# Kernel tuning notes

Measured on AMD Instinct MI355X. Metric: run time of the kernel, lower is better.

## Reference

```python
import jax, jax.numpy as jnp
import numpy as np

N_HEADS = 16
THETA = 10000.0

def rotate_half(x):
    x1, x2 = jnp.split(x, 2, axis=-1)
    return jnp.concatenate((-x2, x1), axis=-1)

def setup_inputs() -> dict:
    key = jax.random.key(0)
    k1, k2, k3 = jax.random.split(key, 3)
    B, T, C = 4, 2048, 2048
    x = jax.random.normal(k1, (B, T, C), dtype=jnp.float32)
    # torch Linear weights: y = x @ W.T
    wqkv = jax.random.normal(k2, (3 * C, C), dtype=jnp.float32) * (1.0 / np.sqrt(C))
    w_out = jax.random.normal(k3, (C, C), dtype=jnp.float32) * (1.0 / np.sqrt(C))
    return {"x": x, "wqkv": wqkv, "w_out": w_out}

def reference(x, wqkv, w_out):
    B, T, C = x.shape
    H = N_HEADS
    hd = C // H
    scale = 1.0 / np.sqrt(hd)

    qkv = x @ wqkv.T                               # [B, T, 3C]
    q, k, v = jnp.split(qkv, 3, axis=-1)
    q = q.reshape(B, T, H, hd).transpose(0, 2, 1, 3)  # [B, H, T, hd]
    k = k.reshape(B, T, H, hd).transpose(0, 2, 1, 3)
    v = v.reshape(B, T, H, hd).transpose(0, 2, 1, 3)

    # rotary embedding (kv_len == T, no cache)
    inv_freq = 1.0 / (THETA ** (jnp.arange(0, hd, 2, dtype=jnp.float32) / hd))
    t = jnp.arange(T, dtype=jnp.float32)
    freqs = jnp.einsum("i,j->ij", t, inv_freq)     # [T, hd/2]
    emb = jnp.concatenate((freqs, freqs), axis=-1) # [T, hd]
    cos = jnp.cos(emb)[None, None, :, :]
    sin = jnp.sin(emb)[None, None, :, :]
    q = q * cos + rotate_half(q) * sin
    k = k * cos + rotate_half(k) * sin

    scores = jnp.einsum("bhqd,bhkd->bhqk", q, k) * scale
    causal = jnp.triu(jnp.ones((T, T), dtype=bool), k=1)
    scores = jnp.where(causal[None, None], -jnp.inf, scores)
    attn = jax.nn.softmax(scores, axis=-1)
    out = jnp.einsum("bhqk,bhkd->bhqd", attn, v)   # [B, H, T, hd]
    out = out.transpose(0, 2, 1, 3).reshape(B, T, C)
    output = out @ w_out.T
    return (output, k, v)
```

## Files before the change

### kernel.cpp

```cpp
#include <hip/hip_runtime.h>

#define B_ 4
#define T_ 2048
#define C_ 2048
#define H_ 16
#define HD_ 128
#define BT_ (B_*T_)
#define N3_ (3*C_)

typedef unsigned short u16;
typedef unsigned int u32;
using short8 = __attribute__((ext_vector_type(8))) short;
using f32x4  = __attribute__((ext_vector_type(4))) float;

__device__ __forceinline__ u16 f2bf(float f) {
  union { float f; u32 u; } v; v.f = f;
  u32 r = v.u + 0x7FFFu + ((v.u >> 16) & 1u);
  return (u16)(r >> 16);
}
__device__ __forceinline__ float bf2f(u16 u) {
  union { u32 u; float f; } v; v.u = ((u32)u) << 16;
  return v.f;
}
__device__ __forceinline__ void gload_lds16(const void* g, void* l) {
  __builtin_amdgcn_global_load_lds((const __attribute__((address_space(1))) void*)g,
                                   (__attribute__((address_space(3))) void*)l, 16, 0, 0);
}

__global__ __launch_bounds__(256) void cast_f2b_kernel(const float* __restrict__ in,
                                                       u16* __restrict__ out, int n4) {
  int i = blockIdx.x * 256 + threadIdx.x;
  if (i >= n4) return;
  float4 v = ((const float4*)in)[i];
  ushort4 o;
  o.x = f2bf(v.x); o.y = f2bf(v.y); o.z = f2bf(v.z); o.w = f2bf(v.w);
  ((ushort4*)out)[i] = o;
}

__global__ __launch_bounds__(256) void rope_table_kernel(float* __restrict__ cosb,
                                                         float* __restrict__ sinb) {
  int i = blockIdx.x * 256 + threadIdx.x;
  int t = i >> 6, d = i & 63;
  float inv = powf(10000.0f, -(float)d / 64.0f);
  float ang = (float)t * inv;
  cosb[i] = cosf(ang);
  sinb[i] = sinf(ang);
}

__global__ __launch_bounds__(256) void rope_apply_kernel(const u16* __restrict__ qkv,
    const float* __restrict__ cosb, const float* __restrict__ sinb,
    u16* __restrict__ qb, u16* __restrict__ kbb,
    float* __restrict__ kout, float* __restrict__ vout) {
  int gid = blockIdx.x * 256 + threadIdx.x;
  int d = gid & 63;
  int h = (gid >> 6) & 15;
  int t = (gid >> 10) & 2047;
  int b = gid >> 21;
  const u16* row = qkv + (size_t)(b * T_ + t) * N3_;
  int base = h * HD_ + d;
  const float SCALE = 0.08838834764831845f;
  float q0 = bf2f(row[base]);
  float q1 = bf2f(row[base + 64]);
  float k0 = bf2f(row[C_ + base]);
  float k1 = bf2f(row[C_ + base + 64]);
  float v0 = bf2f(row[2*C_ + base]);
  float v1 = bf2f(row[2*C_ + base + 64]);
  float c = cosb[t * 64 + d], s = sinb[t * 64 + d];
  size_t o = ((size_t)((b * H_ + h) * T_ + t)) * HD_ + d;
  qb[o]        = f2bf((q0 * c - q1 * s) * SCALE);
  qb[o + 64]   = f2bf((q1 * c + q0 * s) * SCALE);
  float kr0 = k0 * c - k1 * s;
  float kr1 = k1 * c + k0 * s;
  kout[o]      = kr0;
  kout[o + 64] = kr1;
  kbb[o]       = f2bf(kr0);
  kbb[o + 64]  = f2bf(kr1);
  vout[o]      = v0;
  vout[o + 64] = v1;
}

__global__ __launch_bounds__(256) void vt_kernel(const u16* __restrict__ qkvb,
                                                 u16* __restrict__ vtb) {
  __shared__ u16 tile[64][72];
  int bid = blockIdx.x;
  int dh = bid & 1, tt = (bid >> 1) & 31, bh = bid >> 6;
  int b = bh >> 4, h = bh & 15;
  int tid = threadIdx.x;
  int tr = tid >> 2, tc = tid & 3;
  const u16* src = qkvb + (size_t)(b*T_ + tt*64 + tr) * N3_ + 2*C_ + h*HD_ + dh*64 + tc*16;
  short8 v0 = *(const short8*)src;
  short8 v1 = *(const short8*)(src + 8);
  #pragma unroll
  for (int j = 0; j < 8; ++j) {
    tile[tr][tc*16 + j]     = (u16)v0[j];
    tile[tr][tc*16 + 8 + j] = (u16)v1[j];
  }
  __syncthreads();
  int dr = tid >> 2, c2 = tid & 3;
  short8 o0, o1;
  #pragma unroll
  for (int j = 0; j < 8; ++j) {
    o0[j] = (short)tile[c2*16 + j][dr];
    o1[j] = (short)tile[c2*16 + 8 + j][dr];
  }
  u16* dst = vtb + ((size_t)bh * HD_ + dh*64 + dr) * T_ + tt*64 + c2*16;
  *(short8*)dst = o0;
  *(short8*)(dst + 8) = o1;
}

template<int OUT_BF16>
__global__ __launch_bounds__(512, 2) void gemm8p_kernel(const u16* __restrict__ A,
    const u16* __restrict__ Bw, void* __restrict__ Cout, int M, int N, int K, int ntx) {
  extern __shared__ u16 ldsx[];
  int lin = blockIdx.x;
  int cpx = gridDim.x >> 3;
  int wg = (lin & 7) * cpx + (lin >> 3);
  int mtile = wg / ntx, ntile = wg - mtile * ntx;
  int tid = threadIdx.x, w = tid >> 6, l = tid & 63;
  int lr = l & 15, lg = l >> 4;
  int wr = w >> 2, wc = w & 3;
  const u16* Abase = A + (size_t)mtile * 256 * K;
  const u16* Bbase = Bw + (size_t)ntile * 256 * K;

  int goff[2], ldsoff[2];
  #pragma unroll
  for (int j = 0; j < 2; ++j) {
    int s = (j*8 + w)*64 + l;
    int row = (s >> 5)*8 + (s & 7);
    int c = (s & 31) >> 3;
    goff[j] = row * K + c*8;
    ldsoff[j] = (j*8 + w) * 512;
  }
  int bbyte[4], abyte[2][4];
  #pragma unroll
  for (int n = 0; n < 4; ++n) {
    int r = wc*64 + n*16 + lr;
    bbyte[n] = ((r & ~7) << 6) + (lg << 7) + ((r & 7) << 4);
  }
  #pragma unroll
  for (int mq = 0; mq < 2; ++mq)
    #pragma unroll
    for (int m = 0; m < 4; ++m) {
      int r = wr*128 + mq*64 + m*16 + lr;
      abyte[mq][m] = ((r & ~7) << 6) + (lg << 7) + ((r & 7) << 4);
    }

  f32x4 acc[8][4];
  #pragma unroll
  for (int mi = 0; mi < 8; ++mi)
    #pragma unroll
    for (int n = 0; n < 4; ++n) acc[mi][n] = (f32x4){0.f,0.f,0.f,0.f};

  const int NT = K >> 5;
  #pragma unroll
  for (int t0 = 0; t0 < 3; ++t0) {
    const u16* ga = Abase + t0*32;
    const u16* gb = Bbase + t0*32;
    u16* la = ldsx + (size_t)t0 * 16384;
    #pragma unroll
    for (int j = 0; j < 2; ++j) gload_lds16(ga + goff[j], la + ldsoff[j]);
    #pragma unroll
    for (int j = 0; j < 2; ++j) gload_lds16(gb + goff[j], la + 8192 + ldsoff[j]);
  }
  asm volatile("s_waitcnt vmcnt(8)" ::: "memory");
  __builtin_amdgcn_s_barrier();

  for (int t = 0; t < NT; ++t) {
    const char* Al = (const char*)(ldsx + (size_t)(t & 3) * 16384);
    const char* Bl = Al + 16384;
    int tp = t + 3;
    bool st = tp < NT;
    u16* lp = ldsx + (size_t)(tp & 3) * 16384;
    if (st) {
      const u16* ga = Abase + tp*32;
      #pragma unroll
      for (int j = 0; j < 2; ++j) gload_lds16(ga + goff[j], lp + ldsoff[j]);
    }
    short8 bf[4], af[4];
    #pragma unroll
    for (int n = 0; n < 4; ++n) bf[n] = *(const short8*)(Bl + bbyte[n]);
    #pragma unroll
    for (int m = 0; m < 4; ++m) af[m] = *(const short8*)(Al + abyte[0][m]);
    __builtin_amdgcn_s_setprio(1);
    #pragma unroll
    for (int m = 0; m < 4; ++m)
      #pragma unroll
      for (int n = 0; n < 4; ++n)
        acc[m][n] = __builtin_amdgcn_mfma_f32_16x16x32_bf16(af[m], bf[n], acc[m][n], 0, 0, 0);
    __builtin_amdgcn_s_setprio(0);
    __builtin_amdgcn_s_barrier();
    if (st) {
      const u16* gb = Bbase + tp*32;
      #pragma unroll
      for (int j = 0; j < 2; ++j) gload_lds16(gb + goff[j], lp + 8192 + ldsoff[j]);
    }
    #pragma unroll
    for (int m = 0; m < 4; ++m) af[m] = *(const short8*)(Al + abyte[1][m]);
    __builtin_amdgcn_s_setprio(1);
    #pragma unroll
    for (int m = 0; m < 4; ++m)
      #pragma unroll
      for (int n = 0; n < 4; ++n)
        acc[4+m][n] = __builtin_amdgcn_mfma_f32_16x16x32_bf16(af[m], bf[n], acc[4+m][n], 0, 0, 0);
    __builtin_amdgcn_s_setprio(0);
    if (t + 1 < NT) {
      if (t + 3 < NT)      asm volatile("s_waitcnt vmcnt(8)" ::: "memory");
      else if (t + 2 < NT) asm volatile("s_waitcnt vmcnt(4)" ::: "memory");
      else                 asm volatile("s_waitcnt vmcnt(0)" ::: "memory");
    }
    __builtin_amdgcn_s_barrier();
  }
  #pragma unroll
  for (int mi = 0; mi < 8; ++mi)
    #pragma unroll
    for (int n = 0; n < 4; ++n)
      #pragma unroll
      for (int r = 0; r < 4; ++r) {
        int grow = mtile*256 + wr*128 + mi*16 + lg*4 + r;
        int gcol = ntile*256 + wc*64 + n*16 + lr;
        float v = acc[mi][n][r];
        if (OUT_BF16) ((u16*)Cout)[(size_t)grow * N + gcol] = f2bf(v);
        else          ((float*)Cout)[(size_t)grow * N + gcol] = v;
      }
}

struct TileSt {
  short8 aq[4];
  f32x4 oacc[8];
  float m_run[4];
  float l_run[4];
};

__device__ __forceinline__ void stage_kv(const u16* kpl, const u16* vpl, int kt,
                                         u16* Kd, u16* Vd, int w, int l) {
  const u16* kTile = kpl + (size_t)kt * 64 * HD_;
  int ktOff = kt * 64;
  #pragma unroll
  for (int j = 0; j < 4; ++j) {
    int s = (j*4 + w)*64 + l;
    int g = s ^ ((s >> 4) & 7);
    gload_lds16(kTile + (g >> 4)*HD_ + (g & 15)*8, (char*)Kd + (j*4 + w)*1024);
    int g2 = s ^ ((s >> 3) & 7);
    gload_lds16(vpl + (size_t)(g2 >> 3)*T_ + ktOff + (g2 & 7)*8, (char*)Vd + (j*4 + w)*1024);
  }
}

__device__ __forceinline__ void attn_tile(TileSt& st, const u16* Kl, const u16* Vl,
                                          char* Pw, bool diag, int lr, int lg, int w) {
  f32x4 s_acc[4];
  #pragma unroll
  for (int ct = 0; ct < 4; ++ct) s_acc[ct] = (f32x4){0.f, 0.f, 0.f, 0.f};
  __builtin_amdgcn_s_setprio(1);
  #pragma unroll
  for (int kg = 0; kg < 4; ++kg) {
    #pragma unroll
    for (int ct = 0; ct < 4; ++ct) {
      int krow = ct*16 + lr;
      int kbyte = (krow*256 + (kg*32 + lg*8)*2) ^ ((krow & 7) << 4);
      short8 bk = *(const short8*)((const char*)Kl + kbyte);
      s_acc[ct] = __builtin_amdgcn_mfma_f32_16x16x32_bf16(st.aq[kg], bk, s_acc[ct], 0, 0, 0);
    }
  }
  __builtin_amdgcn_s_setprio(0);
  float p[4][4];
  #pragma unroll
  for (int ct = 0; ct < 4; ++ct)
    #pragma unroll
    for (int r = 0; r < 4; ++r) {
      float sv = s_acc[ct][r];
      if (diag && (ct*16 + lr) > (w*16 + lg*4 + r)) sv = -INFINITY;
      p[ct][r] = sv;
    }
  float fac[4];
  #pragma unroll
  for (int r = 0; r < 4; ++r) {
    float mx = fmaxf(fmaxf(p[0][r], p[1][r]), fmaxf(p[2][r], p[3][r]));
    #pragma unroll
    for (int off = 1; off < 16; off <<= 1) mx = fmaxf(mx, __shfl_xor(mx, off));
    float mn = fmaxf(st.m_run[r], mx);
    fac[r] = __expf(st.m_run[r] - mn);
    st.m_run[r] = mn;
    float ls = 0.f;
    #pragma unroll
    for (int ct = 0; ct < 4; ++ct) { float pv = __expf(p[ct][r] - mn); p[ct][r] = pv; ls += pv; }
    #pragma unroll
    for (int off = 1; off < 16; off <<= 1) ls += __shfl_xor(ls, off);
    st.l_run[r] = st.l_run[r] * fac[r] + ls;
  }
  #pragma unroll
  for (int dt = 0; dt < 8; ++dt)
    #pragma unroll
    for (int r = 0; r < 4; ++r) st.oacc[dt][r] *= fac[r];
  #pragma unroll
  for (int ct = 0; ct < 4; ++ct)
    #pragma unroll
    for (int r = 0; r < 4; ++r) {
      int prow = lg*4 + r;
      int pb = (prow*128 + (ct*16 + lr)*2) ^ ((prow & 7) << 4);
      *(u16*)(Pw + pb) = f2bf(p[ct][r]);
    }
  asm volatile("s_waitcnt lgkmcnt(0)" ::: "memory");
  __builtin_amdgcn_sched_barrier(0);
  short8 pa[2];
  #pragma unroll
  for (int kk = 0; kk < 2; ++kk) {
    int pb = (lr*128 + (kk*32 + lg*8)*2) ^ ((lr & 7) << 4);
    pa[kk] = *(const short8*)(Pw + pb);
  }
  __builtin_amdgcn_s_setprio(1);
  #pragma unroll
  for (int dt = 0; dt < 8; ++dt) {
    #pragma unroll
    for (int kk = 0; kk < 2; ++kk) {
      int vrow = dt*16 + lr;
      int vbyte = (vrow*128 + (kk*32 + lg*8)*2) ^ ((vrow & 7) << 4);
      short8 bv = *(const short8*)((const char*)Vl + vbyte);
      st.oacc[dt] = __builtin_amdgcn_mfma_f32_16x16x32_bf16(pa[kk], bv, st.oacc[dt], 0, 0, 0);
    }
  }
  __builtin_amdgcn_s_setprio(0);
}

__device__ __forceinline__ void write_out(TileSt& st, u16* __restrict__ ao,
                                          int b, int h, int qbase, int lr, int lg, int w) {
  float invl[4];
  #pragma unroll
  for (int r = 0; r < 4; ++r) invl[r] = 1.0f / st.l_run[r];
  #pragma unroll
  for (int dt = 0; dt < 8; ++dt)
    #pragma unroll
    for (int r = 0; r < 4; ++r) {
      int t = qbase + w*16 + lg*4 + r;
      int col = h*HD_ + dt*16 + lr;
      ao[(size_t)(b * T_ + t) * C_ + col] = f2bf(st.oacc[dt][r] * invl[r]);
    }
}

__global__ __launch_bounds__(256, 2) void attn_kernel(const u16* __restrict__ qb,
    const u16* __restrict__ kb, const u16* __restrict__ vtb, u16* __restrict__ ao) {
  __shared__ u16 Kl[2][64 * 128];
  __shared__ u16 Vl[2][128 * 64];
  __shared__ u16 Pl[4][16 * 64];
  int bid0 = blockIdx.x;
  int bid = (bid0 & 7) * 128 + (bid0 >> 3);
  int bh = bid >> 4, pr = bid & 15;
  int lo = pr, hi = 31 - pr;
  int b = bh >> 4, h = bh & 15;
  int tid = threadIdx.x, w = tid >> 6, l = tid & 63;
  int lr = l & 15, lg = l >> 4;
  const u16* qptr = qb + (size_t)bh * T_ * HD_;
  const u16* kpl  = kb + (size_t)bh * T_ * HD_;
  const u16* vpl  = vtb + (size_t)bh * HD_ * T_;
  char* Pw = (char*)&Pl[w][0];

  TileSt stL, stH;
  #pragma unroll
  for (int kg = 0; kg < 4; ++kg) {
    stL.aq[kg] = *(const short8*)(qptr + (size_t)(lo*64 + w*16 + lr) * HD_ + kg*32 + lg*8);
    stH.aq[kg] = *(const short8*)(qptr + (size_t)(hi*64 + w*16 + lr) * HD_ + kg*32 + lg*8);
  }
  #pragma unroll
  for (int dt = 0; dt < 8; ++dt) {
    stL.oacc[dt] = (f32x4){0.f, 0.f, 0.f, 0.f};
    stH.oacc[dt] = (f32x4){0.f, 0.f, 0.f, 0.f};
  }
  #pragma unroll
  for (int r = 0; r < 4; ++r) {
    stL.m_run[r] = -INFINITY; stH.m_run[r] = -INFINITY;
    stL.l_run[r] = 0.f;       stH.l_run[r] = 0.f;
  }

  stage_kv(kpl, vpl, 0, &Kl[0][0], &Vl[0][0], w, l);
  __syncthreads();
  int cur = 0;
  for (int kt = 0; kt <= hi; ++kt) {
    if (kt < hi) stage_kv(kpl, vpl, kt + 1, &Kl[cur ^ 1][0], &Vl[cur ^ 1][0], w, l);
    attn_tile(stH, &Kl[cur][0], &Vl[cur][0], Pw, kt == hi, lr, lg, w);
    if (kt <= lo) attn_tile(stL, &Kl[cur][0], &Vl[cur][0], Pw, kt == lo, lr, lg, w);
    __syncthreads();
    cur ^= 1;
  }
  write_out(stH, ao, b, h, hi*64, lr, lg, w);
  write_out(stL, ao, b, h, lo*64, lr, lg, w);
}

extern "C" void kernel_launch(void* const* d_in, const int* in_sizes, int n_in,
                              void* d_out, int out_size, void* d_ws, size_t ws_size,
                              hipStream_t stream) {
  const float* x     = (const float*)d_in[0];
  const float* wqkv  = (const float*)d_in[1];
  const float* w_out = (const float*)d_in[2];
  float* out = (float*)d_out;

  char* ws = (char*)d_ws;
  size_t off = 0;
  u16* xb    = (u16*)(ws + off); off += (size_t)BT_ * C_ * 2;
  u16* wqkvb = (u16*)(ws + off); off += (size_t)N3_ * C_ * 2;
  u16* woutb = (u16*)(ws + off); off += (size_t)C_ * C_ * 2;
  u16* qkvb  = (u16*)(ws + off); off += (size_t)BT_ * N3_ * 2;
  u16* qbf   = (u16*)(ws + off); off += (size_t)BT_ * C_ * 2;
  u16* aob   = (u16*)(ws + off); off += (size_t)BT_ * C_ * 2;
  u16* kbb   = (u16*)(ws + off); off += (size_t)BT_ * C_ * 2;
  u16* vtb   = (u16*)(ws + off); off += (size_t)BT_ * C_ * 2;
  float* cosb = (float*)(ws + off); off += (size_t)T_ * 64 * 4;
  float* sinb = (float*)(ws + off); off += (size_t)T_ * 64 * 4;

  float* kout = out + (size_t)BT_ * C_;
  float* vout = out + 2 * (size_t)BT_ * C_;

  hipFuncSetAttribute((const void*)gemm8p_kernel<1>,
                      hipFuncAttributeMaxDynamicSharedMemorySize, 131072);
  hipFuncSetAttribute((const void*)gemm8p_kernel<0>,
                      hipFuncAttributeMaxDynamicSharedMemorySize, 131072);

  cast_f2b_kernel<<<(BT_*C_/4)/256, 256, 0, stream>>>(x, xb, BT_*C_/4);
  cast_f2b_kernel<<<(N3_*C_/4)/256, 256, 0, stream>>>(wqkv, wqkvb, N3_*C_/4);
  cast_f2b_kernel<<<(C_*C_/4)/256, 256, 0, stream>>>(w_out, woutb, C_*C_/4);
  rope_table_kernel<<<(T_*64)/256, 256, 0, stream>>>(cosb, sinb);
  gemm8p_kernel<1><<<(N3_/256)*(BT_/256), 512, 131072, stream>>>(xb, wqkvb, qkvb, BT_, N3_, C_, N3_/256);
  rope_apply_kernel<<<(B_*T_*H_*64)/256, 256, 0, stream>>>(qkvb, cosb, sinb, qbf, kbb, kout, vout);
  vt_kernel<<<B_*H_*(T_/64)*2, 256, 0, stream>>>(qkvb, vtb);
  attn_kernel<<<B_*H_*16, 256, 0, stream>>>(qbf, kbb, vtb, aob);
  gemm8p_kernel<0><<<(C_/256)*(BT_/256), 512, 131072, stream>>>(aob, woutb, out, BT_, C_, C_, C_/256);
}
```

Measured before the change: 572.6 us.

## Prefetch next K-tile LDS fragments into registers and drop mid-loop barrier

```diff
diff --git a/kernel.cpp b/kernel.cpp
--- a/kernel.cpp
+++ b/kernel.cpp
@@ -162,53 +162,67 @@
     #pragma unroll
     for (int j = 0; j < 2; ++j) gload_lds16(gb + goff[j], la + 8192 + ldsoff[j]);
   }
-  asm volatile("s_waitcnt vmcnt(8)" ::: "memory");
+  asm volatile("s_waitcnt vmcnt(4)" ::: "memory");
   __builtin_amdgcn_s_barrier();
 
+  short8 bf[4], af0[4];
+  {
+    const char* Al0 = (const char*)ldsx;
+    #pragma unroll
+    for (int n = 0; n < 4; ++n) bf[n] = *(const short8*)(Al0 + 16384 + bbyte[n]);
+    #pragma unroll
+    for (int m = 0; m < 4; ++m) af0[m] = *(const short8*)(Al0 + abyte[0][m]);
+  }
+
+  #pragma unroll 2
   for (int t = 0; t < NT; ++t) {
-    const char* Al = (const char*)(ldsx + (size_t)(t & 3) * 16384);
-    const char* Bl = Al + 16384;
+    const char* Al  = (const char*)(ldsx + (size_t)(t & 3) * 16384);
+    const char* Aln = (const char*)(ldsx + (size_t)((t+1) & 3) * 16384);
     int tp = t + 3;
     bool st = tp < NT;
     u16* lp = ldsx + (size_t)(tp & 3) * 16384;
+    short8 af1[4], bfn[4], afn[4];
     if (st) {
       const u16* ga = Abase + tp*32;
       #pragma unroll
       for (int j = 0; j < 2; ++j) gload_lds16(ga + goff[j], lp + ldsoff[j]);
     }
-    short8 bf[4], af[4];
-    #pragma unroll
-    for (int n = 0; n < 4; ++n) bf[n] = *(const short8*)(Bl + bbyte[n]);
-    #pragma unroll
-    for (int m = 0; m < 4; ++m) af[m] = *(const short8*)(Al + abyte[0][m]);
+    #pragma unroll
+    for (int m = 0; m < 4; ++m) af1[m] = *(const short8*)(Al + abyte[1][m]);
     __builtin_amdgcn_s_setprio(1);
     #pragma unroll
     for (int m = 0; m < 4; ++m)
       #pragma unroll
       for (int n = 0; n < 4; ++n)
-        acc[m][n] = __builtin_amdgcn_mfma_f32_16x16x32_bf16(af[m], bf[n], acc[m][n], 0, 0, 0);
+        acc[m][n] = __builtin_amdgcn_mfma_f32_16x16x32_bf16(af0[m], bf[n], acc[m][n], 0, 0, 0);
     __builtin_amdgcn_s_setprio(0);
-    __builtin_amdgcn_s_barrier();
     if (st) {
       const u16* gb = Bbase + tp*32;
       #pragma unroll
       for (int j = 0; j < 2; ++j) gload_lds16(gb + goff[j], lp + 8192 + ldsoff[j]);
     }
-    #pragma unroll
-    for (int m = 0; m < 4; ++m) af[m] = *(const short8*)(Al + abyte[1][m]);
+    if (t + 1 < NT) {
+      #pragma unroll
+      for (int n = 0; n < 4; ++n) bfn[n] = *(const short8*)(Aln + 16384 + bbyte[n]);
+      #pragma unroll
+      for (int m = 0; m < 4; ++m) afn[m] = *(const short8*)(Aln + abyte[0][m]);
+    }
     __builtin_amdgcn_s_setprio(1);
     #pragma unroll
     for (int m = 0; m < 4; ++m)
       #pragma unroll
       for (int n = 0; n < 4; ++n)
-        acc[4+m][n] = __builtin_amdgcn_mfma_f32_16x16x32_bf16(af[m], bf[n], acc[4+m][n], 0, 0, 0);
+        acc[4+m][n] = __builtin_amdgcn_mfma_f32_16x16x32_bf16(af1[m], bf[n], acc[4+m][n], 0, 0, 0);
     __builtin_amdgcn_s_setprio(0);
+    if (t >= NT - 3) { asm volatile("s_waitcnt vmcnt(0)" ::: "memory"); }
+    else             { asm volatile("s_waitcnt vmcnt(4)" ::: "memory"); }
+    __builtin_amdgcn_s_barrier();
     if (t + 1 < NT) {
-      if (t + 3 < NT)      asm volatile("s_waitcnt vmcnt(8)" ::: "memory");
-      else if (t + 2 < NT) asm volatile("s_waitcnt vmcnt(4)" ::: "memory");
-      else                 asm volatile("s_waitcnt vmcnt(0)" ::: "memory");
-    }
-    __builtin_amdgcn_s_barrier();
+      #pragma unroll
+      for (int n = 0; n < 4; ++n) bf[n] = bfn[n];
+      #pragma unroll
+      for (int m = 0; m < 4; ++m) af0[m] = afn[m];
+    }
   }
   #pragma unroll
   for (int mi = 0; mi < 8; ++mi)
```

After: 577.1 us. No clear change (+0.8%).
